# Kernel optimization log

Measured on AMD Instinct MI355X. Metric: run time of the kernel, lower is better.

## Reference

```python
import jax, jax.numpy as jnp
import numpy as np

B = 256   # batch (bs)
N = 6890  # SMPL vertices
J = 24    # joints (root + 23)
NB = 10   # betas
P = 100   # points per foot plane
PARENTS = np.array([-1,0,0,0,1,2,3,4,5,6,7,8,9,9,9,12,13,14,16,17,18,19,20,21], dtype=np.int64)


def setup_inputs() -> dict:
    key = jax.random.key(0)
    ks = jax.random.split(key, 20)
    v_template = jax.random.normal(ks[0], (N, 3), jnp.float32) * 0.3
    shapedirs = jax.random.normal(ks[1], (N, 3, NB), jnp.float32) * 0.01
    Jr = jax.random.uniform(ks[2], (J, N), jnp.float32)
    J_regressor = Jr / Jr.sum(axis=1, keepdims=True)
    lw = jax.random.uniform(ks[3], (N, J), jnp.float32)
    lbs_weights = lw / lw.sum(axis=1, keepdims=True)
    betas = jnp.concatenate([jnp.ones((1, 1), jnp.float32),
                             jax.random.normal(ks[4], (1, NB), jnp.float32) * 0.5], axis=1)
    return dict(
        v_template=v_template, shapedirs=shapedirs, J_regressor=J_regressor,
        lbs_weights=lbs_weights, betas=betas,
        body_pose_wo_foot=jax.random.normal(ks[5], (B, 57), jnp.float32) * 0.2,
        r_back_foot_pose=jax.random.normal(ks[6], (B, 3), jnp.float32) * 0.2,
        r_front_foot_pose=jax.random.normal(ks[7], (B,), jnp.float32) * 0.2,
        l_back_foot_pose=jax.random.normal(ks[8], (B, 3), jnp.float32) * 0.2,
        l_front_foot_pose=jax.random.normal(ks[9], (B,), jnp.float32) * 0.2,
        transl=jax.random.normal(ks[10], (B, 3), jnp.float32) * 0.1,
        global_orient=jax.random.normal(ks[11], (B, 3), jnp.float32) * 0.2,
        init_plane_back_l=jax.random.normal(ks[12], (B, P, 3), jnp.float32) * 0.1,
        init_plane_front_l=jax.random.normal(ks[13], (B, P, 3), jnp.float32) * 0.1,
        init_plane_back_r=jax.random.normal(ks[14], (B, P, 3), jnp.float32) * 0.1,
        init_plane_front_r=jax.random.normal(ks[15], (B, P, 3), jnp.float32) * 0.1,
        parents=jnp.asarray(PARENTS),
        foot_back_l_ids=jax.random.randint(ks[16], (P,), 0, N),
        foot_back_r_ids=jax.random.randint(ks[17], (P,), 0, N),
        foot_front_l_ids=jax.random.randint(ks[18], (P,), 0, N),
        foot_front_r_ids=jax.random.randint(ks[19], (P,), 0, N),
    )


def _rodrigues(rot_vecs):
    # rot_vecs: [M,3] axis-angle -> [M,3,3] rotation matrices (matches SMPL batch_rodrigues)
    angle = jnp.linalg.norm(rot_vecs + 1e-8, axis=1, keepdims=True)  # [M,1]
    rot_dir = rot_vecs / angle
    cos = jnp.cos(angle)[..., None]  # [M,1,1]
    sin = jnp.sin(angle)[..., None]
    rx, ry, rz = rot_dir[:, 0], rot_dir[:, 1], rot_dir[:, 2]
    zeros = jnp.zeros_like(rx)
    K = jnp.stack([zeros, -rz, ry, rz, zeros, -rx, -ry, rx, zeros], axis=1).reshape(-1, 3, 3)
    I = jnp.eye(3, dtype=rot_vecs.dtype)
    return I + sin * K + (1.0 - cos) * jnp.matmul(K, K)


def _forward(v_template, shapedirs, J_regressor, lbs_weights, betas,
             body_pose_wo_foot, r_back_foot_pose, r_front_foot_pose,
             l_back_foot_pose, l_front_foot_pose, transl, global_orient,
             init_plane_back_l, init_plane_front_l, init_plane_back_r, init_plane_front_r,
             ids):
    Bn = body_pose_wo_foot.shape[0]
    dt = v_template.dtype
    # --- update_shape ---
    blend = jnp.einsum('bl,mkl->bmk', betas[:, 1:], shapedirs)            # [1,N,3]
    v_shaped = (v_template[None] + blend) * betas[:, 0][:, None, None]    # [1,N,3]
    J_shaped = jnp.einsum('bik,ji->bjk', v_shaped, J_regressor)           # [1,J,3]
    # --- assemble full pose (foot-joint splicing) ---
    z2 = jnp.zeros((Bn, 2), dt)
    body_pose = jnp.concatenate([
        body_pose_wo_foot[:, :18],              # joints 1..6
        l_back_foot_pose,                       # joint 7
        r_back_foot_pose,                       # joint 8
        body_pose_wo_foot[:, 18:21],            # joint 9
        l_front_foot_pose[:, None], z2,         # joint 10 (x only)
        r_front_foot_pose[:, None], z2,         # joint 11 (x only)
        body_pose_wo_foot[:, 21:]], axis=1)     # joints 12..23
    full_pose = jnp.concatenate([global_orient, body_pose], axis=1)      # [B,72]
    rot = _rodrigues(full_pose.reshape(-1, 3)).reshape(Bn, J, 3, 3)
    # --- batch_rigid_transform ---
    joints = jnp.broadcast_to(J_shaped, (Bn, J, 3))
    rel = jnp.concatenate([joints[:, :1], joints[:, 1:] - joints[:, PARENTS[1:]]], axis=1)
    top = jnp.concatenate([rot, rel[..., None]], axis=-1)                 # [B,J,3,4]
    bottom = jnp.broadcast_to(jnp.array([0., 0., 0., 1.], dt), (Bn, J, 1, 4))
    T_loc = jnp.concatenate([top, bottom], axis=2)                        # [B,J,4,4]
    chain = [T_loc[:, 0]]
    for i in range(1, J):  # fixed 24-joint kinematic chain
        chain.append(chain[int(PARENTS[i])] @ T_loc[:, i])
    transforms = jnp.stack(chain, axis=1)                                 # [B,J,4,4]
    J_transformed = transforms[..., :3, 3]
    init_bone = jnp.einsum('bjmn,bjn->bjm', transforms[..., :3, :3], joints)
    A = transforms.at[..., :3, 3].add(-init_bone)                         # relative transforms
    # --- LBS skinning ---
    T = jnp.einsum('vj,bjmn->bvmn', lbs_weights, A)                       # [B,N,4,4]
    verts = jnp.einsum('bvmn,vn->bvm', T[:, :, :3, :3], v_shaped[0]) + T[:, :, :3, 3] + transl[:, None]
    # --- foot planes ---
    def _plane(idx, init):
        Tp = T[:, idx]                                                    # [B,P,4,4]
        return jnp.einsum('bpmn,bpn->bpm', Tp[:, :, :3, :3], init) + Tp[:, :, :3, 3]
    bl, fl, br, fr = ids
    v_plane = jnp.concatenate([
        _plane(bl, init_plane_back_l), _plane(fl, init_plane_front_l),
        _plane(br, init_plane_back_r), _plane(fr, init_plane_front_r)], axis=1) + transl[:, None]
    return verts, J_transformed, v_plane


def reference(v_template, shapedirs, J_regressor, lbs_weights, betas,
              body_pose_wo_foot, r_back_foot_pose, r_front_foot_pose,
              l_back_foot_pose, l_front_foot_pose, transl, global_orient,
              init_plane_back_l, init_plane_front_l, init_plane_back_r, init_plane_front_r,
              parents, foot_back_l_ids, foot_back_r_ids, foot_front_l_ids, foot_front_r_ids):
    ids = (foot_back_l_ids, foot_front_l_ids, foot_back_r_ids, foot_front_r_ids)
    return _forward(v_template, shapedirs, J_regressor, lbs_weights, betas,
                    body_pose_wo_foot, r_back_foot_pose, r_front_foot_pose,
                    l_back_foot_pose, l_front_foot_pose, transl, global_orient,
                    init_plane_back_l, init_plane_front_l, init_plane_back_r, init_plane_front_r,
                    ids)
```

## Files before the change

### kernel.cpp

```cpp
#include <hip/hip_runtime.h>
#include <stdint.h>

#define NV 6890
#define NJ 24
#define NB_ 256
#define NP 100
#define MP 6912

#define OUT_JT   5291520
#define OUT_PLN  5309952

#define O_JP 0
#define O_A  576
#define O_PW 74304
#define O_WT 169984
#define O_AT 833536

typedef unsigned short u16;
typedef unsigned int u32;
typedef __attribute__((ext_vector_type(8))) short bf16x8;
typedef __attribute__((ext_vector_type(4))) float f32x4;

__device__ __forceinline__ u16 f2bf(float f) {
    u32 u = __float_as_uint(f);
    u += 0x7FFFu + ((u >> 16) & 1u);
    return (u16)(u >> 16);
}

__constant__ int c_par[24] = {-1,0,0,0,1,2,3,4,5,6,7,8,9,9,9,12,13,14,16,17,18,19,20,21};

struct Params {
    const float *vt, *sd, *jreg, *lw, *betas, *bpwf, *rback, *rfront,
                *lback, *lfront, *transl, *gor, *ip_bl, *ip_fl, *ip_br, *ip_fr;
    const int *ids_bl, *ids_fl, *ids_br, *ids_fr;
    float* ws;
    u16* wsu;
    float* out;
};

__global__ __launch_bounds__(256) void k_d1(Params P) {
    int bx = blockIdx.x, tid = threadIdx.x;
    if (bx < 27) {
        int v = bx * 256 + tid;
        u16 buf[96];
        if (v < NV) {
            float be[11];
#pragma unroll
            for (int l = 0; l < 11; ++l) be[l] = P.betas[l];
            const float* sr = P.sd + (size_t)v * 30;
            const float* vr = P.vt + (size_t)v * 3;
            float vs[3];
#pragma unroll
            for (int n = 0; n < 3; ++n) {
                float acc = vr[n];
#pragma unroll
                for (int l = 0; l < 10; ++l) acc += be[1 + l] * sr[n * 10 + l];
                vs[n] = acc * be[0];
            }
            const float* wr = P.lw + (size_t)v * 24;
#pragma unroll
            for (int j = 0; j < 24; ++j) {
                float w = wr[j];
                buf[j*4+0] = f2bf(w * vs[0]);
                buf[j*4+1] = f2bf(w * vs[1]);
                buf[j*4+2] = f2bf(w * vs[2]);
                buf[j*4+3] = f2bf(w);
            }
        } else {
#pragma unroll
            for (int m = 0; m < 96; ++m) buf[m] = 0;
        }
        uint4* dst = (uint4*)(P.wsu + O_WT + (size_t)v * 96);
        const uint4* src = (const uint4*)buf;
#pragma unroll
        for (int m = 0; m < 12; ++m) dst[m] = src[m];
        return;
    }
    {
        int idx = bx - 27;
        int j = idx >> 3, sl = idx & 7;
        int i0 = sl * 862, i1 = (i0 + 862 < NV) ? i0 + 862 : NV;
        float b0 = P.betas[0];
        float be[10];
#pragma unroll
        for (int l = 0; l < 10; ++l) be[l] = P.betas[1 + l];
        float s0 = 0.f, s1 = 0.f, s2 = 0.f;
        for (int i = i0 + tid; i < i1; i += 256) {
            float w = P.jreg[(size_t)j * NV + i];
            const float* sr = P.sd + (size_t)i * 30;
            const float* vr = P.vt + (size_t)i * 3;
            float c0 = vr[0], c1 = vr[1], c2 = vr[2];
#pragma unroll
            for (int l = 0; l < 10; ++l) {
                c0 += be[l] * sr[l];
                c1 += be[l] * sr[10 + l];
                c2 += be[l] * sr[20 + l];
            }
            s0 += w * (c0 * b0); s1 += w * (c1 * b0); s2 += w * (c2 * b0);
        }
        __shared__ float r0[256], r1[256], r2[256];
        r0[tid] = s0; r1[tid] = s1; r2[tid] = s2;
        __syncthreads();
        for (int off = 128; off > 0; off >>= 1) {
            if (tid < off) { r0[tid] += r0[tid+off]; r1[tid] += r1[tid+off]; r2[tid] += r2[tid+off]; }
            __syncthreads();
        }
        if (tid == 0) {
            P.ws[O_JP + (j*8 + sl)*3 + 0] = r0[0];
            P.ws[O_JP + (j*8 + sl)*3 + 1] = r1[0];
            P.ws[O_JP + (j*8 + sl)*3 + 2] = r2[0];
        }
    }
}

__global__ __launch_bounds__(256) void k_d2(Params P) {
    int bx = blockIdx.x, tid = threadIdx.x;
    if (bx >= NB_) {
        int q = (bx - NB_) * 256 + tid;
        if (q < 9600) {
            int rr = q / 24, j = q - 24 * rr;
            int plane = rr / 100, p = rr - 100 * plane;
            const int* ids = (plane == 0) ? P.ids_bl : (plane == 1) ? P.ids_fl
                           : (plane == 2) ? P.ids_br : P.ids_fr;
            P.ws[O_PW + q] = P.lw[(size_t)ids[p] * 24 + j];
        }
        return;
    }
    int b = bx;
    __shared__ float js[72];
    __shared__ float sT[24][12];
    __shared__ float sJ[24][3];
    if (tid < 72) {
        int j = tid / 3, cc = tid - 3 * j;
        float a = 0.f;
#pragma unroll
        for (int s = 0; s < 8; ++s) a += P.ws[O_JP + (j*8 + s)*3 + cc];
        js[tid] = a;
    }
    __syncthreads();
    int j = tid;
    if (j < 24) {
        float px, py, pz;
        const float* bp = P.bpwf;
        if (j == 0)      { px = P.gor[b*3];   py = P.gor[b*3+1];   pz = P.gor[b*3+2]; }
        else if (j <= 6) { int o = b*57 + 3*(j-1); px = bp[o]; py = bp[o+1]; pz = bp[o+2]; }
        else if (j == 7) { px = P.lback[b*3]; py = P.lback[b*3+1]; pz = P.lback[b*3+2]; }
        else if (j == 8) { px = P.rback[b*3]; py = P.rback[b*3+1]; pz = P.rback[b*3+2]; }
        else if (j == 9) { int o = b*57 + 18;     px = bp[o]; py = bp[o+1]; pz = bp[o+2]; }
        else if (j == 10){ px = P.lfront[b];  py = 0.f; pz = 0.f; }
        else if (j == 11){ px = P.rfront[b];  py = 0.f; pz = 0.f; }
        else             { int o = b*57 + 21 + 3*(j-12); px = bp[o]; py = bp[o+1]; pz = bp[o+2]; }
        float ax = px + 1e-8f, ay = py + 1e-8f, az = pz + 1e-8f;
        float ang = sqrtf(ax*ax + ay*ay + az*az);
        float inv = 1.0f / ang;
        float dx = px * inv, dy = py * inv, dz = pz * inv;
        float c = cosf(ang), s = sinf(ang), t = 1.0f - c;
        sJ[j][0] = js[j*3]; sJ[j][1] = js[j*3+1]; sJ[j][2] = js[j*3+2];
        int p = c_par[j];
        float rx = sJ[j][0], ry = sJ[j][1], rz = sJ[j][2];
        if (p >= 0) { rx -= js[p*3]; ry -= js[p*3+1]; rz -= js[p*3+2]; }
        sT[j][0] = 1.f - t*(dy*dy + dz*dz);
        sT[j][1] = -s*dz + t*dx*dy;
        sT[j][2] =  s*dy + t*dx*dz;
        sT[j][3] = rx;
        sT[j][4] =  s*dz + t*dx*dy;
        sT[j][5] = 1.f - t*(dx*dx + dz*dz);
        sT[j][6] = -s*dx + t*dy*dz;
        sT[j][7] = ry;
        sT[j][8] = -s*dy + t*dx*dz;
        sT[j][9] =  s*dx + t*dy*dz;
        sT[j][10]= 1.f - t*(dx*dx + dy*dy);
        sT[j][11]= rz;
    }
    __syncthreads();
    if (j < 24) {
        int path[12]; int d = 0; int cur = j;
        while (cur >= 0) { path[d++] = cur; cur = c_par[cur]; }
        float g[12];
        int r = path[d - 1];
#pragma unroll
        for (int m = 0; m < 12; ++m) g[m] = sT[r][m];
        for (int i = d - 2; i >= 0; --i) {
            int n = path[i];
            float h[12];
#pragma unroll
            for (int row = 0; row < 3; ++row) {
                float a0 = g[row*4+0], a1 = g[row*4+1], a2 = g[row*4+2], a3 = g[row*4+3];
                h[row*4+0] = a0*sT[n][0] + a1*sT[n][4] + a2*sT[n][8];
                h[row*4+1] = a0*sT[n][1] + a1*sT[n][5] + a2*sT[n][9];
                h[row*4+2] = a0*sT[n][2] + a1*sT[n][6] + a2*sT[n][10];
                h[row*4+3] = a0*sT[n][3] + a1*sT[n][7] + a2*sT[n][11] + a3;
            }
#pragma unroll
            for (int m = 0; m < 12; ++m) g[m] = h[m];
        }
        size_t jo = (size_t)OUT_JT + ((size_t)b * 24 + j) * 3;
        P.out[jo+0] = g[3]; P.out[jo+1] = g[7]; P.out[jo+2] = g[11];
        float jx = sJ[j][0], jy = sJ[j][1], jz = sJ[j][2];
        float Av[12];
        Av[0]=g[0]; Av[1]=g[1]; Av[2]=g[2];   Av[3] = g[3]  - (g[0]*jx + g[1]*jy + g[2]*jz);
        Av[4]=g[4]; Av[5]=g[5]; Av[6]=g[6];   Av[7] = g[7]  - (g[4]*jx + g[5]*jy + g[6]*jz);
        Av[8]=g[8]; Av[9]=g[9]; Av[10]=g[10]; Av[11]= g[11] - (g[8]*jx + g[9]*jy + g[10]*jz);
        float* Ab = P.ws + O_A + ((size_t)b * 24 + j) * 12;
#pragma unroll
        for (int m = 0; m < 12; ++m) Ab[m] = Av[m];
        u16* at = P.wsu + O_AT;
#pragma unroll
        for (int m = 0; m < 3; ++m)
#pragma unroll
            for (int n = 0; n < 4; ++n)
                at[(size_t)(b*3 + m) * 96 + j*4 + n] = f2bf(Av[m*4 + n]);
    }
}

__global__ __launch_bounds__(256) void k_d3(Params P) {
    if (blockIdx.y < 12) {
        __shared__ float ltile[64][66];
        const u16* wt = P.wsu + O_WT;
        const u16* at = P.wsu + O_AT;
        int tid = threadIdx.x;
        int lane = tid & 63;
        int wave = tid >> 6;
        int row_in = lane & 15, quad = lane >> 4;
        int v0 = blockIdx.x * 64 + wave * 16;
        int c0 = blockIdx.y * 64;

        f32x4 acc0 = {0.f,0.f,0.f,0.f}, acc1 = acc0, acc2 = acc0, acc3 = acc0;
#pragma unroll
        for (int kc = 0; kc < 96; kc += 32) {
            bf16x8 a  = *(const bf16x8*)(wt + (size_t)(v0 + row_in) * 96 + kc + quad * 8);
            bf16x8 b0 = *(const bf16x8*)(at + (size_t)(c0 +  0 + row_in) * 96 + kc + quad * 8);
            bf16x8 b1 = *(const bf16x8*)(at + (size_t)(c0 + 16 + row_in) * 96 + kc + quad * 8);
            bf16x8 b2 = *(const bf16x8*)(at + (size_t)(c0 + 32 + row_in) * 96 + kc + quad * 8);
            bf16x8 b3 = *(const bf16x8*)(at + (size_t)(c0 + 48 + row_in) * 96 + kc + quad * 8);
            acc0 = __builtin_amdgcn_mfma_f32_16x16x32_bf16(a, b0, acc0, 0, 0, 0);
            acc1 = __builtin_amdgcn_mfma_f32_16x16x32_bf16(a, b1, acc1, 0, 0, 0);
            acc2 = __builtin_amdgcn_mfma_f32_16x16x32_bf16(a, b2, acc2, 0, 0, 0);
            acc3 = __builtin_amdgcn_mfma_f32_16x16x32_bf16(a, b3, acc3, 0, 0, 0);
        }
        int vbase = wave * 16 + quad * 4;
#pragma unroll
        for (int s = 0; s < 4; ++s) {
            f32x4 acc = (s == 0) ? acc0 : (s == 1) ? acc1 : (s == 2) ? acc2 : acc3;
#pragma unroll
            for (int r = 0; r < 4; ++r)
                ltile[vbase + r][s * 16 + row_in] = acc[r];
        }
        __syncthreads();
        int vblk = blockIdx.x * 64;
        int bstart = c0 / 3;
        int bend = (c0 + 63) / 3;
        for (int b = bstart; b <= bend; ++b) {
            if (tid < 192) {
                int vl = tid / 3, m = tid - 3 * (tid / 3);
                int cl = b * 3 + m - c0;
                int v = vblk + vl;
                if (cl >= 0 && cl < 64 && v < NV)
                    P.out[((size_t)b * NV + v) * 3 + m] = ltile[vl][cl] + P.transl[b * 3 + m];
            }
        }
        return;
    }
    for (int idx = blockIdx.x * 256 + threadIdx.x; idx < NB_ * 400; idx += 108 * 256) {
        int b = idx / 400;
        int rr = idx - 400 * b;
        const float* w  = P.ws + O_PW + rr * 24;
        const float* Ab = P.ws + O_A + (size_t)b * 288;
        float T[12];
#pragma unroll
        for (int m = 0; m < 12; ++m) T[m] = 0.f;
#pragma unroll
        for (int j = 0; j < NJ; ++j) {
            float wj = w[j];
#pragma unroll
            for (int m = 0; m < 12; ++m) T[m] += wj * Ab[j * 12 + m];
        }
        int plane = rr / 100, p = rr - 100 * plane;
        const float* ip = (plane == 0) ? P.ip_bl : (plane == 1) ? P.ip_fl
                        : (plane == 2) ? P.ip_br : P.ip_fr;
        size_t io = ((size_t)b * NP + p) * 3;
        float vx = ip[io+0], vy = ip[io+1], vz = ip[io+2];
        float ox = T[0]*vx + T[1]*vy + T[2]*vz  + T[3]  + P.transl[b*3+0];
        float oy = T[4]*vx + T[5]*vy + T[6]*vz  + T[7]  + P.transl[b*3+1];
        float oz = T[8]*vx + T[9]*vy + T[10]*vz + T[11] + P.transl[b*3+2];
        size_t o = (size_t)OUT_PLN + (size_t)idx * 3;
        P.out[o+0] = ox; P.out[o+1] = oy; P.out[o+2] = oz;
    }
}

extern "C" void kernel_launch(void* const* d_in, const int* in_sizes, int n_in,
                              void* d_out, int out_size, void* d_ws, size_t ws_size,
                              hipStream_t stream) {
    Params P;
    P.vt     = (const float*)d_in[0];
    P.sd     = (const float*)d_in[1];
    P.jreg   = (const float*)d_in[2];
    P.lw     = (const float*)d_in[3];
    P.betas  = (const float*)d_in[4];
    P.bpwf   = (const float*)d_in[5];
    P.rback  = (const float*)d_in[6];
    P.rfront = (const float*)d_in[7];
    P.lback  = (const float*)d_in[8];
    P.lfront = (const float*)d_in[9];
    P.transl = (const float*)d_in[10];
    P.gor    = (const float*)d_in[11];
    P.ip_bl  = (const float*)d_in[12];
    P.ip_fl  = (const float*)d_in[13];
    P.ip_br  = (const float*)d_in[14];
    P.ip_fr  = (const float*)d_in[15];
    P.ids_bl = (const int*)d_in[17];
    P.ids_br = (const int*)d_in[18];
    P.ids_fl = (const int*)d_in[19];
    P.ids_fr = (const int*)d_in[20];
    P.ws  = (float*)d_ws;
    P.wsu = (u16*)d_ws;
    P.out = (float*)d_out;

    k_d1<<<dim3(27 + 192), 256, 0, stream>>>(P);
    k_d2<<<dim3(NB_ + 38), 256, 0, stream>>>(P);
    k_d3<<<dim3(108, 13), 256, 0, stream>>>(P);
}
```

Measured before the change: 145.9 us.

## Merge first two kernels using inter-block release/acquire flags

```diff
diff --git a/kernel.cpp b/kernel.cpp
--- a/kernel.cpp
+++ b/kernel.cpp
@@ -6,6 +6,7 @@
 #define NB_ 256
 #define NP 100
 #define MP 6912
+#define MAGIC 0x13579BDF
 
 #define OUT_JT   5291520
 #define OUT_PLN  5309952
@@ -13,6 +14,7 @@
 #define O_JP 0
 #define O_A  576
 #define O_PW 74304
+#define O_FL 83904
 #define O_WT 169984
 #define O_AT 833536
 
@@ -38,7 +40,7 @@
     float* out;
 };
 
-__global__ __launch_bounds__(256) void k_d1(Params P) {
+__global__ __launch_bounds__(256, 2) void k_dA(Params P) {
     int bx = blockIdx.x, tid = threadIdx.x;
     if (bx < 27) {
         int v = bx * 256 + tid;
@@ -76,7 +78,7 @@
         for (int m = 0; m < 12; ++m) dst[m] = src[m];
         return;
     }
-    {
+    if (bx < 219) {
         int idx = bx - 27;
         int j = idx >> 3, sl = idx & 7;
         int i0 = sl * 862, i1 = (i0 + 862 < NV) ? i0 + 862 : NV;
@@ -106,27 +108,36 @@
             __syncthreads();
         }
         if (tid == 0) {
-            P.ws[O_JP + (j*8 + sl)*3 + 0] = r0[0];
-            P.ws[O_JP + (j*8 + sl)*3 + 1] = r1[0];
-            P.ws[O_JP + (j*8 + sl)*3 + 2] = r2[0];
-        }
-    }
-}
-
-__global__ __launch_bounds__(256) void k_d2(Params P) {
-    int bx = blockIdx.x, tid = threadIdx.x;
-    if (bx >= NB_) {
-        int q = (bx - NB_) * 256 + tid;
-        if (q < 9600) {
-            int rr = q / 24, j = q - 24 * rr;
-            int plane = rr / 100, p = rr - 100 * plane;
-            const int* ids = (plane == 0) ? P.ids_bl : (plane == 1) ? P.ids_fl
-                           : (plane == 2) ? P.ids_br : P.ids_fr;
-            P.ws[O_PW + q] = P.lw[(size_t)ids[p] * 24 + j];
+            P.ws[O_JP + idx*3 + 0] = r0[0];
+            P.ws[O_JP + idx*3 + 1] = r1[0];
+            P.ws[O_JP + idx*3 + 2] = r2[0];
+            __threadfence();
+            __hip_atomic_store((int*)P.ws + O_FL + idx, MAGIC,
+                               __ATOMIC_RELEASE, __HIP_MEMORY_SCOPE_AGENT);
         }
         return;
     }
-    int b = bx;
+    int b = bx - 219;
+    {
+        if (tid < 38) {
+            int q = b * 38 + tid;
+            if (q < 9600) {
+                int rr = q / 24, j = q - 24 * rr;
+                int plane = rr / 100, p = rr - 100 * plane;
+                const int* ids = (plane == 0) ? P.ids_bl : (plane == 1) ? P.ids_fl
+                               : (plane == 2) ? P.ids_br : P.ids_fr;
+                P.ws[O_PW + q] = P.lw[(size_t)ids[p] * 24 + j];
+            }
+        }
+    }
+    if (tid < 192) {
+        const int* fl = (const int*)P.ws + O_FL;
+        while (__hip_atomic_load(fl + tid, __ATOMIC_ACQUIRE,
+                                 __HIP_MEMORY_SCOPE_AGENT) != MAGIC) {
+            __builtin_amdgcn_s_sleep(2);
+        }
+    }
+    __syncthreads();
     __shared__ float js[72];
     __shared__ float sT[24][12];
     __shared__ float sJ[24][3];
@@ -316,7 +327,6 @@
     P.wsu = (u16*)d_ws;
     P.out = (float*)d_out;
 
-    k_d1<<<dim3(27 + 192), 256, 0, stream>>>(P);
-    k_d2<<<dim3(NB_ + 38), 256, 0, stream>>>(P);
+    k_dA<<<dim3(475), 256, 0, stream>>>(P);
     k_d3<<<dim3(108, 13), 256, 0, stream>>>(P);
 }
```

After: 195.3 us. 1.34x slower.
